# Optimization experiments

Measured on AMD Instinct MI355X. Metric: run time of the kernel, lower is better.

Reference implementation:

```python
import jax, jax.numpy as jnp
import numpy as np
import math

B_TOPK = 8  # self.B
NEG = -1e9  # numerically-equivalent stand-in for float('-inf') mask


def setup_inputs() -> dict:
    key = jax.random.key(0)
    ks = jax.random.split(key, 12)
    b, s, d, d_low = 4, 2048, 128, 16
    sc = 1.0 / math.sqrt(d)
    return {
        "queries": jax.random.normal(ks[0], (b, s, d), jnp.float32),
        "keys": jax.random.normal(ks[1], (b, s, d), jnp.float32),
        "values": jax.random.normal(ks[2], (b, s, d), jnp.float32),
        "valid_lens": jax.random.randint(ks[3], (b, s), 0, s, jnp.int32),
        "Wq_low": jax.random.normal(ks[4], (d, d_low), jnp.float32) * sc,
        "bq_low": jnp.zeros((d_low,), jnp.float32),
        "Wk_low": jax.random.normal(ks[5], (d, d_low), jnp.float32) * sc,
        "bk_low": jnp.zeros((d_low,), jnp.float32),
        "Wq_high": jax.random.normal(ks[6], (d, d_low), jnp.float32) * sc,
        "bq_high": jnp.zeros((d_low,), jnp.float32),
        "Wk_high": jax.random.normal(ks[7], (d, d_low), jnp.float32) * sc,
        "bk_high": jnp.zeros((d_low,), jnp.float32),
    }


def reference(queries, keys, values, valid_lens, Wq_low, bq_low, Wk_low, bk_low,
              Wq_high, bq_high, Wk_high, bk_high):
    b, s, d = queries.shape
    d_low = Wq_low.shape[1]
    scale = 1.0 / math.sqrt(d_low)

    # low-rank scores [b, sq, sk]
    q_low = queries @ Wq_low + bq_low
    k_low = keys @ Wk_low + bk_low
    scores_low = jnp.einsum('bqe,bke->bqk', q_low, k_low) * scale

    # mask: scatter -inf at (batch, valid_lens[b,k], k) along dim 1 (as in torch code)
    vl = jnp.clip(valid_lens, 0, s - 1)                      # [b, sk]
    mask = vl[:, None, :] == jnp.arange(s)[None, :, None]    # [b, sq, sk]
    scores_masked = jnp.where(mask, scores_low + NEG, scores_low)

    # top-B keys per query row (over key axis)
    _, topk_idx = jax.lax.top_k(scores_masked, B_TOPK)       # [b, s, B]

    # gather top-B queries/keys per row, project to d_low, rank-d_low correction score
    bi = jnp.arange(b)[:, None, None]
    q_high = queries[bi, topk_idx]                           # [b, s, B, d]
    k_high = keys[bi, topk_idx]                              # [b, s, B, d]
    q_proj = q_high @ Wq_high + bq_high                      # [b, s, B, d_low]
    k_proj = k_high @ Wk_high + bk_high
    score_high = jnp.sum(q_proj * k_proj, axis=-1) * scale   # [b, s, B]

    # scatter corrected scores back into the masked score matrix (dim 2)
    si = jnp.arange(s)[None, :, None]
    corrected = scores_masked.at[bi, si, topk_idx].set(score_high)

    # masked_softmax with valid_lens applies softmax over dim=1
    attn = jax.nn.softmax(corrected, axis=1)
    return jnp.einsum('bqk,bkd->bqd', attn, values)
```

## Files before the change

### kernel.cpp

```cpp
#include <hip/hip_runtime.h>
#include <float.h>
#include <math.h>

#define SEQ 2048
#define NB 4
#define DIM 128
#define DL 16
#define NEGV (-1e9f)
#define TOPK 8

#define QT 128
#define KC 64
#define QCH 64

typedef unsigned long long u64;
typedef __attribute__((ext_vector_type(8))) short short8;
typedef __attribute__((ext_vector_type(4))) float f32x4;

__device__ __forceinline__ int lanes_below(u64 m) {
    return __builtin_amdgcn_mbcnt_hi((unsigned)(m >> 32),
           __builtin_amdgcn_mbcnt_lo((unsigned)m, 0));
}

__device__ __forceinline__ void top8_insert(float* s, float key) {
    #pragma unroll
    for (int i = 0; i < 8; ++i) {
        float a = s[i];
        s[i] = fmaxf(a, key);
        key  = fminf(a, key);
    }
}

__device__ __forceinline__ float top8_merge(float* s) {
    #pragma unroll
    for (int off = 1; off < 64; off <<= 1) {
        float o[8], t[8];
        #pragma unroll
        for (int i = 0; i < 8; ++i)
            o[i] = __shfl_xor(s[i], off, 64);
        #pragma unroll
        for (int i = 0; i < 8; ++i)
            t[i] = fmaxf(s[i], o[7 - i]);
        #pragma unroll
        for (int i = 0; i < 4; ++i) {
            float a = t[i], c = t[i + 4];
            t[i] = fmaxf(a, c); t[i + 4] = fminf(a, c);
        }
        #pragma unroll
        for (int g2 = 0; g2 < 8; g2 += 4) {
            float a = t[g2], c = t[g2 + 2];
            t[g2] = fmaxf(a, c); t[g2 + 2] = fminf(a, c);
            a = t[g2 + 1]; c = t[g2 + 3];
            t[g2 + 1] = fmaxf(a, c); t[g2 + 3] = fminf(a, c);
        }
        #pragma unroll
        for (int g1 = 0; g1 < 8; g1 += 2) {
            float a = t[g1], c = t[g1 + 1];
            t[g1] = fmaxf(a, c); t[g1 + 1] = fminf(a, c);
        }
        #pragma unroll
        for (int i = 0; i < 8; ++i) s[i] = t[i];
    }
    return s[7];
}

__device__ __forceinline__ unsigned bf16_rne(float x) {
    unsigned u = __float_as_uint(x);
    return (u + 0x7FFFu + ((u >> 16) & 1u)) >> 16;
}

__global__ __launch_bounds__(256) void proj_kernel(
    const float* __restrict__ q, const float* __restrict__ k,
    const float* __restrict__ Wql, const float* __restrict__ bql,
    const float* __restrict__ Wkl, const float* __restrict__ bkl,
    const float* __restrict__ Wqh, const float* __restrict__ bqh,
    const float* __restrict__ Wkh, const float* __restrict__ bkh,
    float* __restrict__ q_low, float* __restrict__ k_low,
    float* __restrict__ sh)
{
    __shared__ float Ws[4][DIM * DL];
    __shared__ float rowq[16][DIM];
    __shared__ float rowk[16][DIM];
    int tid = threadIdx.x;
    for (int i = tid; i < DIM * DL; i += 256) {
        Ws[0][i] = Wql[i];
        Ws[1][i] = Wkl[i];
        Ws[2][i] = Wqh[i];
        Ws[3][i] = Wkh[i];
    }
    int r0 = blockIdx.x * 16;
    for (int i = tid; i < 16 * DIM; i += 256) {
        int rr = i >> 7, cc = i & 127;
        rowq[rr][cc] = q[(size_t)(r0 + rr) * DIM + cc];
        rowk[rr][cc] = k[(size_t)(r0 + rr) * DIM + cc];
    }
    __syncthreads();
    int g = tid >> 4;
    int e = tid & 15;
    float aql = 0.f, akl = 0.f, aqh = 0.f, akh = 0.f;
    #pragma unroll 8
    for (int i = 0; i < DIM; ++i) {
        float qv = rowq[g][i], kv = rowk[g][i];
        aql = fmaf(qv, Ws[0][i * DL + e], aql);
        akl = fmaf(kv, Ws[1][i * DL + e], akl);
        aqh = fmaf(qv, Ws[2][i * DL + e], aqh);
        akh = fmaf(kv, Ws[3][i * DL + e], akh);
    }
    int t = r0 + g;
    q_low[(size_t)t * DL + e] = aql + bql[e];
    k_low[(size_t)t * DL + e] = akl + bkl[e];
    float qp = aqh + bqh[e];
    float kp = akh + bkh[e];
    float prod = qp * kp;
    #pragma unroll
    for (int off = 8; off >= 1; off >>= 1)
        prod += __shfl_xor(prod, off, 16);
    if (e == 0) sh[t] = 0.25f * prod;
}

__global__ __launch_bounds__(256) void vsplit_kernel(
    const float* __restrict__ V, unsigned short* __restrict__ VH,
    unsigned short* __restrict__ VL)
{
    __shared__ float T[32][33];
    int kb = blockIdx.x * 32, db = blockIdx.y * 32, b = blockIdx.z;
    int tid = threadIdx.x;
    {
        int r = tid >> 3, cg = tid & 7;
        float4 v = *(const float4*)(V + ((size_t)b * SEQ + kb + r) * DIM + db + cg * 4);
        T[r][cg * 4 + 0] = v.x; T[r][cg * 4 + 1] = v.y;
        T[r][cg * 4 + 2] = v.z; T[r][cg * 4 + 3] = v.w;
    }
    __syncthreads();
    int dr = tid >> 3, kg = tid & 7;
    unsigned h[4], l[4];
    #pragma unroll
    for (int j = 0; j < 4; ++j) {
        float f = T[kg * 4 + j][dr];
        unsigned hi = bf16_rne(f);
        float hf = __uint_as_float(hi << 16);
        unsigned lo = bf16_rne(f - hf);
        h[j] = hi; l[j] = lo;
    }
    size_t o = ((size_t)b * DIM + db + dr) * SEQ + kb + kg * 4;
    *(uint2*)(VH + o) = make_uint2(h[0] | (h[1] << 16), h[2] | (h[3] << 16));
    *(uint2*)(VL + o) = make_uint2(l[0] | (l[1] << 16), l[2] | (l[3] << 16));
}

__global__ __launch_bounds__(256) void score_topk5(
    const float* __restrict__ q_low, const float* __restrict__ k_low,
    const float* __restrict__ sh, const int* __restrict__ valid_lens,
    float* __restrict__ Smat)
{
    __shared__ float KT[2][256 * DL];

    int tid  = threadIdx.x;
    int lane = tid & 63;
    int wv   = tid >> 6;
    int row0 = __builtin_amdgcn_readfirstlane(blockIdx.x * 8 + wv * 2);
    int b    = row0 >> 11;
    int qi0  = row0 & (SEQ - 1);
    int qi1  = qi0 + 1;

    float qv0[16], qv1[16];
    {
        const float* qp0 = q_low + (size_t)row0 * DL;
        #pragma unroll
        for (int e = 0; e < 16; ++e) { qv0[e] = qp0[e]; qv1[e] = qp0[DL + e]; }
    }

    const float4* kb4 = (const float4*)(k_low + (size_t)b * SEQ * DL);
    const int*    vlb = valid_lens + (size_t)b * SEQ;
    const float*  shb = sh + (size_t)b * SEQ;
    float* Srow0 = Smat + (size_t)row0 * SEQ;
    float* Srow1 = Srow0 + SEQ;

    float s0[8], s1[8];
    #pragma unroll
    for (int i = 0; i < 8; ++i) { s0[i] = -FLT_MAX; s1[i] = -FLT_MAX; }

    float4 stg[4];
    #pragma unroll
    for (int i = 0; i < 4; ++i) stg[i] = kb4[tid + i * 256];
    {
        float4* d = (float4*)KT[0];
        #pragma unroll
        for (int i = 0; i < 4; ++i) d[tid + i * 256] = stg[i];
    }
    __syncthreads();

    for (int c = 0; c < 8; ++c) {
        if (c < 7) {
            #pragma unroll
            for (int i = 0; i < 4; ++i)
                stg[i] = kb4[(c + 1) * 1024 + tid + i * 256];
        }
        int vli[4];
        #pragma unroll
        for (int j = 0; j < 4; ++j)
            vli[j] = vlb[c * 256 + lane + j * 64];

        const float* Kc = KT[c & 1];
        #pragma unroll
        for (int j = 0; j < 4; ++j) {
            int ccol = lane + j * 64;
            int col  = c * 256 + ccol;
            const float4* kp4 = (const float4*)(Kc + ccol * DL);
            float4 v0 = kp4[0], v1 = kp4[1], v2 = kp4[2], v3 = kp4[3];

            float a0 = 0.f, a1 = 0.f;
            a0 = fmaf(qv0[0],  v0.x, a0); a1 = fmaf(qv1[0],  v0.x, a1);
            a0 = fmaf(qv0[1],  v0.y, a0); a1 = fmaf(qv1[1],  v0.y, a1);
            a0 = fmaf(qv0[2],  v0.z, a0); a1 = fmaf(qv1[2],  v0.z, a1);
            a0 = fmaf(qv0[3],  v0.w, a0); a1 = fmaf(qv1[3],  v0.w, a1);
            a0 = fmaf(qv0[4],  v1.x, a0); a1 = fmaf(qv1[4],  v1.x, a1);
            a0 = fmaf(qv0[5],  v1.y, a0); a1 = fmaf(qv1[5],  v1.y, a1);
            a0 = fmaf(qv0[6],  v1.z, a0); a1 = fmaf(qv1[6],  v1.z, a1);
            a0 = fmaf(qv0[7],  v1.w, a0); a1 = fmaf(qv1[7],  v1.w, a1);
            a0 = fmaf(qv0[8],  v2.x, a0); a1 = fmaf(qv1[8],  v2.x, a1);
            a0 = fmaf(qv0[9],  v2.y, a0); a1 = fmaf(qv1[9],  v2.y, a1);
            a0 = fmaf(qv0[10], v2.z, a0); a1 = fmaf(qv1[10], v2.z, a1);
            a0 = fmaf(qv0[11], v2.w, a0); a1 = fmaf(qv1[11], v2.w, a1);
            a0 = fmaf(qv0[12], v3.x, a0); a1 = fmaf(qv1[12], v3.x, a1);
            a0 = fmaf(qv0[13], v3.y, a0); a1 = fmaf(qv1[13], v3.y, a1);
            a0 = fmaf(qv0[14], v3.z, a0); a1 = fmaf(qv1[14], v3.z, a1);
            a0 = fmaf(qv0[15], v3.w, a0); a1 = fmaf(qv1[15], v3.w, a1);
            a0 *= 0.25f; a1 *= 0.25f;

            int v = vli[j];
            v = v < 0 ? 0 : (v > SEQ - 1 ? SEQ - 1 : v);
            if (v == qi0) a0 += NEGV;
            if (v == qi1) a1 += NEGV;
            Srow0[col] = a0;
            Srow1[col] = a1;
            top8_insert(s0, a0);
            top8_insert(s1, a1);
        }
        if (c < 7) {
            float4* d = (float4*)KT[(c + 1) & 1];
            #pragma unroll
            for (int i = 0; i < 4; ++i) d[tid + i * 256] = stg[i];
            __syncthreads();
        }
    }

    float t8[2];
    t8[0] = top8_merge(s0);
    t8[1] = top8_merge(s1);

    for (int r = 0; r < 2; ++r) {
        float* Sr = r ? Srow1 : Srow0;
        float thr = t8[r];
        float sc[32];
        #pragma unroll 8
        for (int j = 0; j < 32; ++j)
            sc[j] = Sr[lane + j * 64];
        int cnt = 0;
        #pragma unroll
        for (int j = 0; j < 32; ++j) {
            cnt += (sc[j] >= thr) ? 1 : 0;
            cnt += (sc[j] >  thr) ? 65536 : 0;
        }
        #pragma unroll
        for (int off = 1; off < 64; off <<= 1)
            cnt += __shfl_xor(cnt, off, 64);
        int c_ge = cnt & 0xFFFF;
        int c_gt = cnt >> 16;

        if (c_ge == 8) {
            #pragma unroll 8
            for (int j = 0; j < 32; ++j) {
                int col = lane + j * 64;
                if (sc[j] >= thr) Sr[col] = shb[col];
            }
        } else {
            int need = 8 - c_gt;
            int total = 0;
            for (int j = 0; j < 32; ++j) {
                int col = lane + j * 64;
                bool eq = (sc[j] == thr);
                u64 bal = __ballot(eq);
                int before = total + lanes_below(bal);
                bool sel = (sc[j] > thr) || (eq && before < need);
                if (sel) Sr[col] = shb[col];
                total += (int)__popcll(bal);
            }
        }
    }
}

__global__ __launch_bounds__(256) void colred_partial(
    const float* __restrict__ Smat, float* __restrict__ pm, float* __restrict__ pl)
{
    int kcol = blockIdx.x * 256 + threadIdx.x;
    int qc = blockIdx.y;
    int b  = blockIdx.z;
    const float* Sp = Smat + (size_t)b * SEQ * SEQ + (size_t)(qc * QCH) * SEQ + kcol;
    float m = -FLT_MAX, l = 0.f;
    #pragma unroll 4
    for (int qq = 0; qq < QCH; ++qq) {
        float v = Sp[(size_t)qq * SEQ];
        float nm = fmaxf(m, v);
        l = l * __expf(m - nm) + __expf(v - nm);
        m = nm;
    }
    pm[((size_t)b * 32 + qc) * SEQ + kcol] = m;
    pl[((size_t)b * 32 + qc) * SEQ + kcol] = l;
}

__global__ __launch_bounds__(256) void colred_final(
    const float* __restrict__ pm, const float* __restrict__ pl,
    float* __restrict__ cmax, float* __restrict__ cinv)
{
    int idx = blockIdx.x * 256 + threadIdx.x;
    int b = idx >> 11, kcol = idx & (SEQ - 1);
    float m = -FLT_MAX, l = 0.f;
    #pragma unroll
    for (int c = 0; c < 32; ++c) {
        float mm = pm[((size_t)b * 32 + c) * SEQ + kcol];
        float ll = pl[((size_t)b * 32 + c) * SEQ + kcol];
        float nm = fmaxf(m, mm);
        l = l * __expf(m - nm) + ll * __expf(mm - nm);
        m = nm;
    }
    cmax[idx] = m;
    cinv[idx] = 1.f / l;
}

__global__ __launch_bounds__(256) void out_mfma(
    const float* __restrict__ Smat, const unsigned short* __restrict__ VH,
    const unsigned short* __restrict__ VL,
    const float* __restrict__ cmax, const float* __restrict__ cinv,
    float* __restrict__ dst, int krange)
{
    __shared__ unsigned int VtH[DIM * 32];
    __shared__ unsigned int VtL[DIM * 32];

    int tid  = threadIdx.x;
    int w    = tid >> 6;
    int lane = tid & 63;
    int ln   = lane & 15;
    int quad = lane >> 4;
    int q0   = blockIdx.x * QT;
    int ksid = blockIdx.y;
    int b    = blockIdx.z;
    int kbeg = ksid * krange;

    const float* Sb = Smat + (size_t)b * SEQ * SEQ;
    const unsigned short* VHb = VH + (size_t)b * DIM * SEQ;
    const unsigned short* VLb = VL + (size_t)b * DIM * SEQ;
    const float* cm = cmax + (size_t)b * SEQ;
    const float* ci = cinv + (size_t)b * SEQ;

    f32x4 acc[2][8];
    #pragma unroll
    for (int mt = 0; mt < 2; ++mt)
        #pragma unroll
        for (int nt = 0; nt < 8; ++nt)
            acc[mt][nt] = (f32x4){0.f, 0.f, 0.f, 0.f};

    int sd0   = tid >> 3;
    int skseg = tid & 7;

    for (int k0 = kbeg; k0 < kbeg + krange; k0 += KC) {
        #pragma unroll
        for (int it = 0; it < 4; ++it) {
            int d = sd0 + it * 32;
            size_t go = (size_t)d * SEQ + k0 + skseg * 8;
            uint4 hv = *(const uint4*)(VHb + go);
            uint4 lv = *(const uint4*)(VLb + go);
            int wa = d * 32 + ((skseg ^ (d & 7)) << 2);
            *(uint4*)&VtH[wa] = hv;
            *(uint4*)&VtL[wa] = lv;
        }

        short8 Ah[2][2], Al[2][2];
        #pragma unroll
        for (int ks = 0; ks < 2; ++ks) {
            int kk = k0 + ks * 32 + quad * 8;
            float4 cma = *(const float4*)(cm + kk);
            float4 cmb = *(const float4*)(cm + kk + 4);
            float4 cia = *(const float4*)(ci + kk);
            float4 cib = *(const float4*)(ci + kk + 4);
            #pragma unroll
            for (int mt = 0; mt < 2; ++mt) {
                const float* Sp = Sb + (size_t)(q0 + w * 32 + mt * 16 + ln) * SEQ + kk;
                float4 sa = *(const float4*)Sp;
                float4 sb = *(const float4*)(Sp + 4);
                float p[8];
                p[0] = __expf(sa.x - cma.x) * cia.x;
                p[1] = __expf(sa.y - cma.y) * cia.y;
                p[2] = __expf(sa.z - cma.z) * cia.z;
                p[3] = __expf(sa.w - cma.w) * cia.w;
                p[4] = __expf(sb.x - cmb.x) * cib.x;
                p[5] = __expf(sb.y - cmb.y) * cib.y;
                p[6] = __expf(sb.z - cmb.z) * cib.z;
                p[7] = __expf(sb.w - cmb.w) * cib.w;
                #pragma unroll
                for (int j = 0; j < 8; ++j) {
                    unsigned hi = bf16_rne(p[j]);
                    float hf = __uint_as_float(hi << 16);
                    unsigned lo = bf16_rne(p[j] - hf);
                    Ah[mt][ks][j] = (short)hi;
                    Al[mt][ks][j] = (short)lo;
                }
            }
        }
        __syncthreads();

        #pragma unroll
        for (int nt = 0; nt < 8; ++nt) {
            int d = nt * 16 + ln;
            #pragma unroll
            for (int ks = 0; ks < 2; ++ks) {
                int kseg = ks * 4 + quad;
                int wa = d * 32 + ((kseg ^ (d & 7)) << 2);
                short8 bh = *(short8*)&VtH[wa];
                short8 bl = *(short8*)&VtL[wa];
                #pragma unroll
                for (int mt = 0; mt < 2; ++mt) {
                    acc[mt][nt] = __builtin_amdgcn_mfma_f32_16x16x32_bf16(
                        Ah[mt][ks], bh, acc[mt][nt], 0, 0, 0);
                    acc[mt][nt] = __builtin_amdgcn_mfma_f32_16x16x32_bf16(
                        Al[mt][ks], bh, acc[mt][nt], 0, 0, 0);
                    acc[mt][nt] = __builtin_amdgcn_mfma_f32_16x16x32_bf16(
                        Ah[mt][ks], bl, acc[mt][nt], 0, 0, 0);
                }
            }
        }
        __syncthreads();
    }

    float* dp = dst + (size_t)ksid * ((size_t)NB * SEQ * DIM)
                    + (size_t)b * SEQ * DIM;
    #pragma unroll
    for (int mt = 0; mt < 2; ++mt) {
        #pragma unroll
        for (int r = 0; r < 4; ++r) {
            float* o = dp + (size_t)(q0 + w * 32 + mt * 16 + quad * 4 + r) * DIM + ln;
            #pragma unroll
            for (int nt = 0; nt < 8; ++nt)
                o[nt * 16] = acc[mt][nt][r];
        }
    }
}

__global__ __launch_bounds__(256) void reduce_kernel(
    const float* __restrict__ part, float* __restrict__ out, int ksplit)
{
    int idx = blockIdx.x * 256 + threadIdx.x;
    const float4* p = (const float4*)part;
    float4 a = p[idx];
    for (int s = 1; s < ksplit; ++s) {
        float4 q = p[(size_t)idx + (size_t)s * 262144];
        a.x += q.x; a.y += q.y; a.z += q.z; a.w += q.w;
    }
    ((float4*)out)[idx] = a;
}

extern "C" void kernel_launch(void* const* d_in, const int* in_sizes, int n_in,
                              void* d_out, int out_size, void* d_ws, size_t ws_size,
                              hipStream_t stream)
{
    const float* queries = (const float*)d_in[0];
    const float* keys    = (const float*)d_in[1];
    const float* values  = (const float*)d_in[2];
    const int*   valid   = (const int*)d_in[3];
    const float* Wql = (const float*)d_in[4];
    const float* bql = (const float*)d_in[5];
    const float* Wkl = (const float*)d_in[6];
    const float* bkl = (const float*)d_in[7];
    const float* Wqh = (const float*)d_in[8];
    const float* bqh = (const float*)d_in[9];
    const float* Wkh = (const float*)d_in[10];
    const float* bkh = (const float*)d_in[11];

    char* ws = (char*)d_ws;
    float* Smat  = (float*)(ws);
    float* q_low = (float*)(ws + 67108864);
    float* k_low = (float*)(ws + 67633152);
    float* sh    = (float*)(ws + 68157440);
    float* cmax  = (float*)(ws + 68190208);
    float* cinv  = (float*)(ws + 68222976);
    unsigned short* VthH = (unsigned short*)(ws + 68255744);
    unsigned short* VthL = (unsigned short*)(ws + 70352896);
    float* pm    = (float*)(ws + 72450048);
    float* pl    = (float*)(ws + 73498624);
    float* part  = (float*)(ws + 72450048);

    const size_t part_off = 72450048;
    const size_t part_sz  = (size_t)NB * SEQ * DIM * 4;
    int ksplit = 1;
    if      (ws_size >= part_off + 8 * part_sz) ksplit = 8;
    else if (ws_size >= part_off + 4 * part_sz) ksplit = 4;
    else if (ws_size >= part_off + 2 * part_sz) ksplit = 2;

    proj_kernel<<<dim3((NB * SEQ) / 16), 256, 0, stream>>>(
        queries, keys, Wql, bql, Wkl, bkl, Wqh, bqh, Wkh, bkh, q_low, k_low, sh);

    vsplit_kernel<<<dim3(SEQ / 32, DIM / 32, NB), 256, 0, stream>>>(
        values, VthH, VthL);

    score_topk5<<<dim3((NB * SEQ) / 8), 256, 0, stream>>>(
        q_low, k_low, sh, valid, Smat);

    colred_partial<<<dim3(SEQ / 256, 32, NB), 256, 0, stream>>>(Smat, pm, pl);

    colred_final<<<dim3((NB * SEQ) / 256), 256, 0, stream>>>(pm, pl, cmax, cinv);

    if (ksplit == 1) {
        out_mfma<<<dim3(SEQ / QT, 1, NB), 256, 0, stream>>>(
            Smat, VthH, VthL, cmax, cinv, (float*)d_out, SEQ);
    } else {
        out_mfma<<<dim3(SEQ / QT, ksplit, NB), 256, 0, stream>>>(
            Smat, VthH, VthL, cmax, cinv, part, SEQ / ksplit);
        reduce_kernel<<<(NB * SEQ * DIM / 4) / 256, 256, 0, stream>>>(
            part, (float*)d_out, ksplit);
    }
}
```

Before: 190.9 us.

## Merge projection and V-split kernels and register-prefetch V tiles in out_mfma

The projection kernel and the V bf16-split kernel are combined into one launch that picks its role from the block index, which saves a launch and lets the two independent jobs run at the same time. In out_mfma, the next V chunk's global loads are issued into registers before the current chunk's compute, so load latency can overlap with the MFMA work. The cost is more register pressure in out_mfma, and the merged kernel's shared memory is sized for the larger projection path.

```diff
diff --git a/kernel.cpp b/kernel.cpp
--- a/kernel.cpp
+++ b/kernel.cpp
@@ -13,6 +13,9 @@
 #define KC 64
 #define QCH 64
 
+#define PROJ_BLOCKS ((NB * SEQ) / 16)
+#define VSPLIT_BLOCKS ((SEQ / 32) * (DIM / 32) * NB)
+
 typedef unsigned long long u64;
 typedef __attribute__((ext_vector_type(8))) short short8;
 typedef __attribute__((ext_vector_type(4))) float f32x4;
@@ -69,82 +72,86 @@
     return (u + 0x7FFFu + ((u >> 16) & 1u)) >> 16;
 }
 
-__global__ __launch_bounds__(256) void proj_kernel(
+__global__ __launch_bounds__(256) void prep_kernel(
     const float* __restrict__ q, const float* __restrict__ k,
+    const float* __restrict__ V,
     const float* __restrict__ Wql, const float* __restrict__ bql,
     const float* __restrict__ Wkl, const float* __restrict__ bkl,
     const float* __restrict__ Wqh, const float* __restrict__ bqh,
     const float* __restrict__ Wkh, const float* __restrict__ bkh,
     float* __restrict__ q_low, float* __restrict__ k_low,
-    float* __restrict__ sh)
-{
-    __shared__ float Ws[4][DIM * DL];
-    __shared__ float rowq[16][DIM];
-    __shared__ float rowk[16][DIM];
+    float* __restrict__ sh,
+    unsigned short* __restrict__ VH, unsigned short* __restrict__ VL)
+{
+    __shared__ float smem[12288];
     int tid = threadIdx.x;
-    for (int i = tid; i < DIM * DL; i += 256) {
-        Ws[0][i] = Wql[i];
-        Ws[1][i] = Wkl[i];
-        Ws[2][i] = Wqh[i];
-        Ws[3][i] = Wkh[i];
-    }
-    int r0 = blockIdx.x * 16;
-    for (int i = tid; i < 16 * DIM; i += 256) {
-        int rr = i >> 7, cc = i & 127;
-        rowq[rr][cc] = q[(size_t)(r0 + rr) * DIM + cc];
-        rowk[rr][cc] = k[(size_t)(r0 + rr) * DIM + cc];
-    }
-    __syncthreads();
-    int g = tid >> 4;
-    int e = tid & 15;
-    float aql = 0.f, akl = 0.f, aqh = 0.f, akh = 0.f;
-    #pragma unroll 8
-    for (int i = 0; i < DIM; ++i) {
-        float qv = rowq[g][i], kv = rowk[g][i];
-        aql = fmaf(qv, Ws[0][i * DL + e], aql);
-        akl = fmaf(kv, Ws[1][i * DL + e], akl);
-        aqh = fmaf(qv, Ws[2][i * DL + e], aqh);
-        akh = fmaf(kv, Ws[3][i * DL + e], akh);
-    }
-    int t = r0 + g;
-    q_low[(size_t)t * DL + e] = aql + bql[e];
-    k_low[(size_t)t * DL + e] = akl + bkl[e];
-    float qp = aqh + bqh[e];
-    float kp = akh + bkh[e];
-    float prod = qp * kp;
-    #pragma unroll
-    for (int off = 8; off >= 1; off >>= 1)
-        prod += __shfl_xor(prod, off, 16);
-    if (e == 0) sh[t] = 0.25f * prod;
-}
-
-__global__ __launch_bounds__(256) void vsplit_kernel(
-    const float* __restrict__ V, unsigned short* __restrict__ VH,
-    unsigned short* __restrict__ VL)
-{
-    __shared__ float T[32][33];
-    int kb = blockIdx.x * 32, db = blockIdx.y * 32, b = blockIdx.z;
-    int tid = threadIdx.x;
-    {
-        int r = tid >> 3, cg = tid & 7;
-        float4 v = *(const float4*)(V + ((size_t)b * SEQ + kb + r) * DIM + db + cg * 4);
-        T[r][cg * 4 + 0] = v.x; T[r][cg * 4 + 1] = v.y;
-        T[r][cg * 4 + 2] = v.z; T[r][cg * 4 + 3] = v.w;
-    }
-    __syncthreads();
-    int dr = tid >> 3, kg = tid & 7;
-    unsigned h[4], l[4];
-    #pragma unroll
-    for (int j = 0; j < 4; ++j) {
-        float f = T[kg * 4 + j][dr];
-        unsigned hi = bf16_rne(f);
-        float hf = __uint_as_float(hi << 16);
-        unsigned lo = bf16_rne(f - hf);
-        h[j] = hi; l[j] = lo;
-    }
-    size_t o = ((size_t)b * DIM + db + dr) * SEQ + kb + kg * 4;
-    *(uint2*)(VH + o) = make_uint2(h[0] | (h[1] << 16), h[2] | (h[3] << 16));
-    *(uint2*)(VL + o) = make_uint2(l[0] | (l[1] << 16), l[2] | (l[3] << 16));
+    int bid = blockIdx.x;
+
+    if (bid < PROJ_BLOCKS) {
+        float* Ws   = smem;
+        float* rowq = smem + 8192;
+        float* rowk = smem + 10240;
+        for (int i = tid; i < DIM * DL; i += 256) {
+            Ws[0 * 2048 + i] = Wql[i];
+            Ws[1 * 2048 + i] = Wkl[i];
+            Ws[2 * 2048 + i] = Wqh[i];
+            Ws[3 * 2048 + i] = Wkh[i];
+        }
+        int r0 = bid * 16;
+        for (int i = tid; i < 16 * DIM; i += 256) {
+            int rr = i >> 7, cc = i & 127;
+            rowq[rr * DIM + cc] = q[(size_t)(r0 + rr) * DIM + cc];
+            rowk[rr * DIM + cc] = k[(size_t)(r0 + rr) * DIM + cc];
+        }
+        __syncthreads();
+        int g = tid >> 4;
+        int e = tid & 15;
+        float aql = 0.f, akl = 0.f, aqh = 0.f, akh = 0.f;
+        #pragma unroll 8
+        for (int i = 0; i < DIM; ++i) {
+            float qv = rowq[g * DIM + i], kv = rowk[g * DIM + i];
+            aql = fmaf(qv, Ws[0 * 2048 + i * DL + e], aql);
+            akl = fmaf(kv, Ws[1 * 2048 + i * DL + e], akl);
+            aqh = fmaf(qv, Ws[2 * 2048 + i * DL + e], aqh);
+            akh = fmaf(kv, Ws[3 * 2048 + i * DL + e], akh);
+        }
+        int t = r0 + g;
+        q_low[(size_t)t * DL + e] = aql + bql[e];
+        k_low[(size_t)t * DL + e] = akl + bkl[e];
+        float qp = aqh + bqh[e];
+        float kp = akh + bkh[e];
+        float prod = qp * kp;
+        #pragma unroll
+        for (int off = 8; off >= 1; off >>= 1)
+            prod += __shfl_xor(prod, off, 16);
+        if (e == 0) sh[t] = 0.25f * prod;
+    } else {
+        int n  = bid - PROJ_BLOCKS;
+        int kb = (n & 63) * 32;
+        int db = ((n >> 6) & 3) * 32;
+        int b  = n >> 8;
+        float (*T)[33] = (float(*)[33])smem;
+        {
+            int r = tid >> 3, cg = tid & 7;
+            float4 v = *(const float4*)(V + ((size_t)b * SEQ + kb + r) * DIM + db + cg * 4);
+            T[r][cg * 4 + 0] = v.x; T[r][cg * 4 + 1] = v.y;
+            T[r][cg * 4 + 2] = v.z; T[r][cg * 4 + 3] = v.w;
+        }
+        __syncthreads();
+        int dr = tid >> 3, kg = tid & 7;
+        unsigned h[4], l[4];
+        #pragma unroll
+        for (int j = 0; j < 4; ++j) {
+            float f = T[kg * 4 + j][dr];
+            unsigned hi = bf16_rne(f);
+            float hf = __uint_as_float(hi << 16);
+            unsigned lo = bf16_rne(f - hf);
+            h[j] = hi; l[j] = lo;
+        }
+        size_t o = ((size_t)b * DIM + db + dr) * SEQ + kb + kg * 4;
+        *(uint2*)(VH + o) = make_uint2(h[0] | (h[1] << 16), h[2] | (h[3] << 16));
+        *(uint2*)(VL + o) = make_uint2(l[0] | (l[1] << 16), l[2] | (l[3] << 16));
+    }
 }
 
 __global__ __launch_bounds__(256) void score_topk5(
@@ -237,7 +244,8 @@
             top8_insert(s1, a1);
         }
         if (c < 7) {
-            float4* d = (float4*)KT[(c + 1) & 1];
+            float* d0 = KT[(c + 1) & 1];
+            float4* d = (float4*)d0;
             #pragma unroll
             for (int i = 0; i < 4; ++i) d[tid + i * 256] = stg[i];
             __syncthreads();
@@ -362,16 +370,31 @@
     int sd0   = tid >> 3;
     int skseg = tid & 7;
 
+    uint4 hreg[4], lreg[4];
+    #pragma unroll
+    for (int it = 0; it < 4; ++it) {
+        int d = sd0 + it * 32;
+        size_t go = (size_t)d * SEQ + kbeg + skseg * 8;
+        hreg[it] = *(const uint4*)(VHb + go);
+        lreg[it] = *(const uint4*)(VLb + go);
+    }
+
     for (int k0 = kbeg; k0 < kbeg + krange; k0 += KC) {
         #pragma unroll
         for (int it = 0; it < 4; ++it) {
             int d = sd0 + it * 32;
-            size_t go = (size_t)d * SEQ + k0 + skseg * 8;
-            uint4 hv = *(const uint4*)(VHb + go);
-            uint4 lv = *(const uint4*)(VLb + go);
             int wa = d * 32 + ((skseg ^ (d & 7)) << 2);
-            *(uint4*)&VtH[wa] = hv;
-            *(uint4*)&VtL[wa] = lv;
+            *(uint4*)&VtH[wa] = hreg[it];
+            *(uint4*)&VtL[wa] = lreg[it];
+        }
+        if (k0 + KC < kbeg + krange) {
+            #pragma unroll
+            for (int it = 0; it < 4; ++it) {
+                int d = sd0 + it * 32;
+                size_t go = (size_t)d * SEQ + (k0 + KC) + skseg * 8;
+                hreg[it] = *(const uint4*)(VHb + go);
+                lreg[it] = *(const uint4*)(VLb + go);
+            }
         }
 
         short8 Ah[2][2], Al[2][2];
@@ -495,11 +518,9 @@
     else if (ws_size >= part_off + 4 * part_sz) ksplit = 4;
     else if (ws_size >= part_off + 2 * part_sz) ksplit = 2;
 
-    proj_kernel<<<dim3((NB * SEQ) / 16), 256, 0, stream>>>(
-        queries, keys, Wql, bql, Wkl, bkl, Wqh, bqh, Wkh, bkh, q_low, k_low, sh);
-
-    vsplit_kernel<<<dim3(SEQ / 32, DIM / 32, NB), 256, 0, stream>>>(
-        values, VthH, VthL);
+    prep_kernel<<<dim3(PROJ_BLOCKS + VSPLIT_BLOCKS), 256, 0, stream>>>(
+        queries, keys, values, Wql, bql, Wkl, bkl, Wqh, bqh, Wkh, bkh,
+        q_low, k_low, sh, VthH, VthL);
 
     score_topk5<<<dim3((NB * SEQ) / 8), 256, 0, stream>>>(
         q_low, k_low, sh, valid, Smat);
```

Result: slower. 208.0 us (+8.9%).

## Double-buffer V tiles in out_mfma with register prefetch of next chunk

Applied to the files above, without the earlier changes.

The V tile loads in out_mfma now use two LDS buffers. The next chunk's global loads are issued into registers before the softmax/exp computation and written to the alternate buffer before the MFMA loop. This removes one barrier per iteration and hides global load latency behind compute, at the cost of doubled LDS usage (64KB) and extra registers, which may reduce occupancy. The KT change in the other kernel is cosmetic.

```diff
diff --git a/kernel.cpp b/kernel.cpp
--- a/kernel.cpp
+++ b/kernel.cpp
@@ -237,7 +237,8 @@
             top8_insert(s1, a1);
         }
         if (c < 7) {
-            float4* d = (float4*)KT[(c + 1) & 1];
+            float* d0 = KT[(c + 1) & 1];
+            float4* d = (float4*)d0;
             #pragma unroll
             for (int i = 0; i < 4; ++i) d[tid + i * 256] = stg[i];
             __syncthreads();
@@ -333,8 +334,8 @@
     const float* __restrict__ cmax, const float* __restrict__ cinv,
     float* __restrict__ dst, int krange)
 {
-    __shared__ unsigned int VtH[DIM * 32];
-    __shared__ unsigned int VtL[DIM * 32];
+    __shared__ unsigned int VtH[2][DIM * 32];
+    __shared__ unsigned int VtL[2][DIM * 32];
 
     int tid  = threadIdx.x;
     int w    = tid >> 6;
@@ -362,16 +363,37 @@
     int sd0   = tid >> 3;
     int skseg = tid & 7;
 
-    for (int k0 = kbeg; k0 < kbeg + krange; k0 += KC) {
-        #pragma unroll
-        for (int it = 0; it < 4; ++it) {
-            int d = sd0 + it * 32;
-            size_t go = (size_t)d * SEQ + k0 + skseg * 8;
-            uint4 hv = *(const uint4*)(VHb + go);
-            uint4 lv = *(const uint4*)(VLb + go);
-            int wa = d * 32 + ((skseg ^ (d & 7)) << 2);
-            *(uint4*)&VtH[wa] = hv;
-            *(uint4*)&VtL[wa] = lv;
+    int nc = krange / KC;
+
+    uint4 hreg[4], lreg[4];
+    #pragma unroll
+    for (int it = 0; it < 4; ++it) {
+        int d = sd0 + it * 32;
+        size_t go = (size_t)d * SEQ + kbeg + skseg * 8;
+        hreg[it] = *(const uint4*)(VHb + go);
+        lreg[it] = *(const uint4*)(VLb + go);
+    }
+    #pragma unroll
+    for (int it = 0; it < 4; ++it) {
+        int d = sd0 + it * 32;
+        int wa = d * 32 + ((skseg ^ (d & 7)) << 2);
+        *(uint4*)&VtH[0][wa] = hreg[it];
+        *(uint4*)&VtL[0][wa] = lreg[it];
+    }
+    __syncthreads();
+
+    for (int cc = 0; cc < nc; ++cc) {
+        int k0  = kbeg + cc * KC;
+        int cur = cc & 1;
+
+        if (cc + 1 < nc) {
+            #pragma unroll
+            for (int it = 0; it < 4; ++it) {
+                int d = sd0 + it * 32;
+                size_t go = (size_t)d * SEQ + (k0 + KC) + skseg * 8;
+                hreg[it] = *(const uint4*)(VHb + go);
+                lreg[it] = *(const uint4*)(VLb + go);
+            }
         }
 
         short8 Ah[2][2], Al[2][2];
@@ -406,7 +428,16 @@
                 }
             }
         }
-        __syncthreads();
+
+        if (cc + 1 < nc) {
+            #pragma unroll
+            for (int it = 0; it < 4; ++it) {
+                int d = sd0 + it * 32;
+                int wa = d * 32 + ((skseg ^ (d & 7)) << 2);
+                *(uint4*)&VtH[cur ^ 1][wa] = hreg[it];
+                *(uint4*)&VtL[cur ^ 1][wa] = lreg[it];
+            }
+        }
 
         #pragma unroll
         for (int nt = 0; nt < 8; ++nt) {
@@ -415,8 +446,8 @@
             for (int ks = 0; ks < 2; ++ks) {
                 int kseg = ks * 4 + quad;
                 int wa = d * 32 + ((kseg ^ (d & 7)) << 2);
-                short8 bh = *(short8*)&VtH[wa];
-                short8 bl = *(short8*)&VtL[wa];
+                short8 bh = *(short8*)&VtH[cur][wa];
+                short8 bl = *(short8*)&VtL[cur][wa];
                 #pragma unroll
                 for (int mt = 0; mt < 2; ++mt) {
                     acc[mt][nt] = __builtin_amdgcn_mfma_f32_16x16x32_bf16(
@@ -428,6 +459,7 @@
                 }
             }
         }
+
         __syncthreads();
     }
 
```

Result: slower. 220.0 us (+15.2%).
